# Performance work log

Hardware: AMD Instinct MI355X
Metric: run time of the kernel (lower is better)

Reference implementation:

```python
import jax, jax.numpy as jnp
import numpy as np

DIM = 512
HEADS = 8
DIM_HEAD = 64
INNER = HEADS * DIM_HEAD
B, N = 2, 2048
EPS = 1e-5


def setup_inputs() -> dict:
    key = jax.random.key(0)
    ks = jax.random.split(key, 7)
    x = jax.random.normal(ks[0], (B, N, DIM), dtype=jnp.float32)
    sph_dist = jax.random.uniform(ks[1], (N, N), dtype=jnp.float32)
    ln_g = jnp.ones((DIM,), jnp.float32) + 0.02 * jax.random.normal(ks[2], (DIM,))
    ln_b = 0.02 * jax.random.normal(ks[3], (DIM,))
    w_qkv = jax.random.normal(ks[4], (DIM, 3 * INNER), dtype=jnp.float32) / np.sqrt(DIM)
    w_out = jax.random.normal(ks[5], (INNER, DIM), dtype=jnp.float32) / np.sqrt(INNER)
    b_out = 0.02 * jax.random.normal(ks[6], (DIM,))
    return {"x": x, "sph_dist": sph_dist, "ln_g": ln_g, "ln_b": ln_b,
            "w_qkv": w_qkv, "w_out": w_out, "b_out": b_out}


def reference(x, sph_dist, ln_g, ln_b, w_qkv, w_out, b_out):
    scale = DIM_HEAD ** -0.5
    # LayerNorm over last dim
    mu = jnp.mean(x, axis=-1, keepdims=True)
    var = jnp.mean(jnp.square(x - mu), axis=-1, keepdims=True)
    xn = (x - mu) * jax.lax.rsqrt(var + EPS) * ln_g + ln_b
    # QKV projection -> [b, h, n, d]
    qkv = xn @ w_qkv  # [b, n, 3*inner]
    q, k, v = jnp.split(qkv, 3, axis=-1)
    split_heads = lambda t: t.reshape(B, N, HEADS, DIM_HEAD).transpose(0, 2, 1, 3)
    q, k, v = split_heads(q), split_heads(k), split_heads(v)
    dots = jnp.einsum('bhid,bhjd->bhij', q, k) * scale  # [b,h,n,n]
    dw = dots * (1.0 + sph_dist[None, None])
    # cross-head normalization: mean/std over head axis (std unbiased, ddof=1)
    m = jnp.mean(dw, axis=1, keepdims=True)
    sd = jnp.sqrt(jnp.sum(jnp.square(dw - m), axis=1, keepdims=True) / (HEADS - 1))
    dw = (dw - m) / sd
    attn = jax.nn.softmax(dw, axis=-1)
    out = jnp.einsum('bhij,bhjd->bhid', attn, v)
    out = out.transpose(0, 2, 1, 3).reshape(B, N, INNER)
    return out @ w_out + b_out
```

## Files before the change

kernel.cpp:

```cpp
#include <hip/hip_runtime.h>
#include <math.h>


typedef __attribute__((ext_vector_type(8))) short bf16x8;
typedef __attribute__((ext_vector_type(8))) unsigned short u16x8;
typedef __attribute__((ext_vector_type(4))) float f32x4;

constexpr int kDim = 512;
constexpr int kN = 2048;
constexpr float kEps = 1e-5f;
constexpr float kLog2e = 1.4426950408889634f;
constexpr float kShift2 = 2.6457513f * 1.4426950408889634f;

constexpr size_t OFF_XN    = 0;
constexpr size_t OFF_WQBT  = 4u << 20;
constexpr size_t OFF_WOHIT = 6u << 20;
constexpr size_t OFF_WOLOT = (6u << 20) + (512u << 10);
constexpr size_t OFF_QB    = 8u << 20;
constexpr size_t OFF_KHI   = 12u << 20;
constexpr size_t OFF_VTHI  = 16u << 20;
constexpr size_t OFF_OP    = 20u << 20;
constexpr size_t OP_STRIDE = 2097152;
constexpr size_t OFF_AOHI  = 0;
constexpr size_t OFF_AOLO  = 8u << 20;

__device__ __forceinline__ unsigned short bf16_rne(float f) {
  unsigned int u = __float_as_uint(f);
  u += 0x7fffu + ((u >> 16) & 1u);
  return (unsigned short)(u >> 16);
}
__device__ __forceinline__ void bf16_split(float x, unsigned short& hi,
                                           unsigned short& lo) {
  unsigned int u = __float_as_uint(x);
  hi = (unsigned short)(u >> 16);
  float r = x - __uint_as_float(u & 0xffff0000u);
  lo = (unsigned short)(__float_as_uint(r) >> 16);
}
__device__ __forceinline__ f32x4 mfma16(bf16x8 a, bf16x8 b, f32x4 c) {
  return __builtin_amdgcn_mfma_f32_16x16x32_bf16(a, b, c, 0, 0, 0);
}

__global__ __launch_bounds__(256) void k_prep(const float* __restrict__ x,
    const float* __restrict__ g, const float* __restrict__ bta,
    const float* __restrict__ wqkv, const float* __restrict__ wout,
    unsigned short* __restrict__ xn, unsigned short* __restrict__ wqbt,
    unsigned short* __restrict__ wohit, unsigned short* __restrict__ wolot) {
  __shared__ unsigned short th[64][72];
  __shared__ unsigned short tl[64][72];
  const int bid = blockIdx.x;
  const int t = threadIdx.x;
  if (bid < 1024) {
    const int row = bid * 4 + (t >> 6);
    const int lane = t & 63;
    const float* xr = x + (size_t)row * kDim + lane * 8;
    float4 a = *(const float4*)xr;
    float4 b = *(const float4*)(xr + 4);
    float s = a.x + a.y + a.z + a.w + b.x + b.y + b.z + b.w;
    float q = a.x*a.x + a.y*a.y + a.z*a.z + a.w*a.w
            + b.x*b.x + b.y*b.y + b.z*b.z + b.w*b.w;
#pragma unroll
    for (int off = 1; off < 64; off <<= 1) {
      s += __shfl_xor(s, off);
      q += __shfl_xor(q, off);
    }
    const float m = s * (1.0f / kDim);
    const float inv = rsqrtf(q * (1.0f / kDim) - m * m + kEps);
    float4 ga = *(const float4*)(g + lane * 8);
    float4 gb = *(const float4*)(g + lane * 8 + 4);
    float4 ba = *(const float4*)(bta + lane * 8);
    float4 bb = *(const float4*)(bta + lane * 8 + 4);
    u16x8 o;
    o[0] = bf16_rne((a.x - m) * inv * ga.x + ba.x);
    o[1] = bf16_rne((a.y - m) * inv * ga.y + ba.y);
    o[2] = bf16_rne((a.z - m) * inv * ga.z + ba.z);
    o[3] = bf16_rne((a.w - m) * inv * ga.w + ba.w);
    o[4] = bf16_rne((b.x - m) * inv * gb.x + bb.x);
    o[5] = bf16_rne((b.y - m) * inv * gb.y + bb.y);
    o[6] = bf16_rne((b.z - m) * inv * gb.z + bb.z);
    o[7] = bf16_rne((b.w - m) * inv * gb.w + bb.w);
    *(u16x8*)(xn + (size_t)row * kDim + lane * 8) = o;
  } else if (bid < 1216) {
    const int tid = bid - 1024;
    const int k0 = (tid / 24) * 64;
    const int n0 = (tid % 24) * 64;
    const int r = t >> 2, c0 = (t & 3) * 16;
    const float* src = wqkv + (size_t)(k0 + r) * 1536 + n0 + c0;
#pragma unroll
    for (int qq = 0; qq < 2; ++qq) {
      float4 v0 = *(const float4*)(src + qq * 8);
      float4 v1 = *(const float4*)(src + qq * 8 + 4);
      u16x8 o;
      o[0] = bf16_rne(v0.x); o[1] = bf16_rne(v0.y);
      o[2] = bf16_rne(v0.z); o[3] = bf16_rne(v0.w);
      o[4] = bf16_rne(v1.x); o[5] = bf16_rne(v1.y);
      o[6] = bf16_rne(v1.z); o[7] = bf16_rne(v1.w);
      *(u16x8*)&th[r][c0 + qq * 8] = o;
    }
    __syncthreads();
#pragma unroll
    for (int qq = 0; qq < 2; ++qq) {
      u16x8 o;
#pragma unroll
      for (int e = 0; e < 8; ++e) o[e] = th[c0 + qq * 8 + e][r];
      *(u16x8*)(wqbt + (size_t)(n0 + r) * 512 + k0 + c0 + qq * 8) = o;
    }
  } else {
    const int tid = bid - 1216;
    const int k0 = (tid >> 3) * 64;
    const int n0 = (tid & 7) * 64;
    const int r = t >> 2, c0 = (t & 3) * 16;
    const float* src = wout + (size_t)(k0 + r) * 512 + n0 + c0;
#pragma unroll
    for (int qq = 0; qq < 2; ++qq) {
      float4 v0 = *(const float4*)(src + qq * 8);
      float4 v1 = *(const float4*)(src + qq * 8 + 4);
      float e8[8] = {v0.x, v0.y, v0.z, v0.w, v1.x, v1.y, v1.z, v1.w};
      u16x8 oh, ol;
#pragma unroll
      for (int e = 0; e < 8; ++e) {
        unsigned short h2, l2;
        bf16_split(e8[e], h2, l2);
        oh[e] = h2;
        ol[e] = l2;
      }
      *(u16x8*)&th[r][c0 + qq * 8] = oh;
      *(u16x8*)&tl[r][c0 + qq * 8] = ol;
    }
    __syncthreads();
#pragma unroll
    for (int qq = 0; qq < 2; ++qq) {
      u16x8 oh, ol;
#pragma unroll
      for (int e = 0; e < 8; ++e) {
        oh[e] = th[c0 + qq * 8 + e][r];
        ol[e] = tl[c0 + qq * 8 + e][r];
      }
      *(u16x8*)(wohit + (size_t)(n0 + r) * 512 + k0 + c0 + qq * 8) = oh;
      *(u16x8*)(wolot + (size_t)(n0 + r) * 512 + k0 + c0 + qq * 8) = ol;
    }
  }
}

__global__ __launch_bounds__(256, 3) void k_gemm_qkv(
    const unsigned short* __restrict__ xn, const unsigned short* __restrict__ wqbt,
    unsigned short* __restrict__ qb, unsigned short* __restrict__ khi,
    unsigned short* __restrict__ vthi) {
  __shared__ unsigned short Ah[64 * 40];
  __shared__ unsigned short Bh[128 * 40];
  __shared__ unsigned short Vt[128 * 72];
  const int t = threadIdx.x;
  const int wv = t >> 6;
  const int lane = t & 63;
  const int col = lane & 15, gq = lane >> 4;
  const int lg = (blockIdx.x & 7) * 96 + (blockIdx.x >> 3);
  const int n0 = (lg % 12) * 128;
  const int m0 = (lg / 12) * 64;
  const int ar = t >> 2, aq = (t & 3) * 8;
  const int bnr = t >> 1, bko = (t & 1) * 16;

  f32x4 acc[8];
#pragma unroll
  for (int bn = 0; bn < 8; ++bn) acc[bn] = (f32x4){0.f, 0.f, 0.f, 0.f};

  for (int k0 = 0; k0 < kDim; k0 += 32) {
    *(u16x8*)&Ah[ar * 40 + aq] =
        *(const u16x8*)(xn + (size_t)(m0 + ar) * kDim + k0 + aq);
    {
      const unsigned short* wr = wqbt + (size_t)(n0 + bnr) * 512 + k0 + bko;
      *(u16x8*)&Bh[bnr * 40 + bko] = *(const u16x8*)(wr);
      *(u16x8*)&Bh[bnr * 40 + bko + 8] = *(const u16x8*)(wr + 8);
    }
    __syncthreads();
    bf16x8 ahf = *(const bf16x8*)&Ah[(wv * 16 + col) * 40 + gq * 8];
#pragma unroll
    for (int bn = 0; bn < 8; ++bn) {
      bf16x8 bhf = *(const bf16x8*)&Bh[(bn * 16 + col) * 40 + gq * 8];
      acc[bn] = mfma16(ahf, bhf, acc[bn]);
    }
    __syncthreads();
  }
  const int which = n0 >> 9;
  if (which < 2) {
    unsigned short* p = (which == 0) ? qb : khi;
#pragma unroll
    for (int r = 0; r < 4; ++r) {
      const int m = m0 + wv * 16 + gq * 4 + r;
      const int bI = m >> 11, nn = m & 2047;
#pragma unroll
      for (int bn = 0; bn < 8; ++bn) {
        const int cc = (n0 & 511) + bn * 16 + col;
        const int hh = cc >> 6, d = cc & 63;
        p[((size_t)(bI * 8 + hh) * kN + nn) * 64 + d] = bf16_rne(acc[bn][r]);
      }
    }
  } else {
#pragma unroll
    for (int bn = 0; bn < 8; ++bn)
#pragma unroll
      for (int r = 0; r < 4; ++r)
        Vt[(bn * 16 + col) * 72 + wv * 16 + gq * 4 + r] = bf16_rne(acc[bn][r]);
    __syncthreads();
    const int cl = t >> 1, mo = (t & 1) * 32;
    const int cc = (n0 & 511) + cl;
    const int hh = cc >> 6, d = cc & 63;
    const int bI = m0 >> 11, ntok = (m0 & 2047) + mo;
    unsigned short* dst = vthi + ((size_t)(bI * 8 + hh) * 64 + d) * kN + ntok;
#pragma unroll
    for (int e = 0; e < 4; ++e)
      *(u16x8*)(dst + e * 8) = *(const u16x8*)&Vt[cl * 72 + mo + e * 8];
  }
}

__global__ __launch_bounds__(512, 2) void k_attn(
    const unsigned short* __restrict__ qb, const unsigned short* __restrict__ khi,
    const unsigned short* __restrict__ vthi,
    float* __restrict__ op, float* __restrict__ lsum, int jLen) {
  constexpr int SSTR = 33;
  __shared__ float Ss[2][512 * SSTR];

  const int t = threadIdx.x;
  const int h = t >> 6;
  const int lane = t & 63;
  const int col = lane & 15;
  const int g = lane >> 4;
  const int lbid = (blockIdx.x & 7) * ((int)gridDim.x >> 3) + (blockIdx.x >> 3);
  const int tileId = lbid & 63;
  const int sId = lbid >> 6;
  const int bI = tileId >> 5;
  const int i0 = (tileId & 31) << 6;
  const int jStart = sId * jLen;
  int jEnd = jStart + jLen;
  if (jEnd > kN) jEnd = kN;
  const int ntile = (jEnd - jStart) >> 5;
  const size_t bh = (size_t)bI * 8 + h;
  float* opart = op + (size_t)sId * OP_STRIDE;

  bf16x8 qhf[4][2];
#pragma unroll
  for (int rb = 0; rb < 4; ++rb) {
    const size_t qoff = (bh * kN + i0 + rb * 16 + col) * 64 + g * 8;
    qhf[rb][0] = *(const bf16x8*)(qb + qoff);
    qhf[rb][1] = *(const bf16x8*)(qb + qoff + 32);
  }
  const unsigned short* kb_h = khi + (bh * kN + col) * 64 + g * 8;
  const unsigned short* vb_h = vthi + (bh * 64 + col) * kN + g * 8;

  const int iN = t >> 3;
  const int jN = (t & 7) * 4;

  f32x4 oacc[4][4];
#pragma unroll
  for (int rb = 0; rb < 4; ++rb)
#pragma unroll
    for (int nf = 0; nf < 4; ++nf) oacc[rb][nf] = (f32x4){0.f, 0.f, 0.f, 0.f};
  float lacc[8] = {0.f, 0.f, 0.f, 0.f, 0.f, 0.f, 0.f, 0.f};

  bf16x8 kh[2][2];
  auto load_k = [&](int j0) {
    const size_t ko = (size_t)j0 * 64;
#pragma unroll
    for (int jf = 0; jf < 2; ++jf)
#pragma unroll
      for (int c = 0; c < 2; ++c)
        kh[jf][c] = *(const bf16x8*)(kb_h + ko + jf * 1024 + c * 32);
  };
  auto qk_tile = [&](int buf) {
#pragma unroll
    for (int rb = 0; rb < 4; ++rb)
#pragma unroll
      for (int jf = 0; jf < 2; ++jf) {
        f32x4 a = (f32x4){0.f, 0.f, 0.f, 0.f};
        a = mfma16(qhf[rb][0], kh[jf][0], a);
        a = mfma16(qhf[rb][1], kh[jf][1], a);
#pragma unroll
        for (int r = 0; r < 4; ++r)
          Ss[buf][(h * 64 + rb * 16 + g * 4 + r) * SSTR + jf * 16 + col] = a[r];
      }
  };

  load_k(jStart);
  qk_tile(0);
  if (ntile > 1) load_k(jStart + 32);
  __syncthreads();

  for (int tt = 0; tt < ntile; ++tt) {
    const int cur = tt & 1;
    const int j0 = jStart + (tt << 5);
    if (tt + 1 < ntile) {
      qk_tile(cur ^ 1);
      if (tt + 2 < ntile) load_k(j0 + 64);
    }
    bf16x8 vhf[4];
#pragma unroll
    for (int nf = 0; nf < 4; ++nf)
      vhf[nf] = *(const bf16x8*)(vb_h + (size_t)(nf * 16) * kN + j0);
    {
      float dv[8][4];
#pragma unroll
      for (int hh = 0; hh < 8; ++hh) {
        float4 v = *(const float4*)&Ss[cur][(hh * 64 + iN) * SSTR + jN];
        dv[hh][0] = v.x; dv[hh][1] = v.y; dv[hh][2] = v.z; dv[hh][3] = v.w;
      }
#pragma unroll
      for (int jj = 0; jj < 4; ++jj) {
        float s = 0.f;
#pragma unroll
        for (int hh = 0; hh < 8; ++hh) s += dv[hh][jj];
        const float mean = s * 0.125f;
        float var = 0.f;
#pragma unroll
        for (int hh = 0; hh < 8; ++hh) {
          float d = dv[hh][jj] - mean;
          var += d * d;
        }
        const float inv2 = rsqrtf(var * (1.0f / 7.0f)) * kLog2e;
        const float base = mean * inv2 + kShift2;
#pragma unroll
        for (int hh = 0; hh < 8; ++hh)
          dv[hh][jj] = __builtin_amdgcn_exp2f(dv[hh][jj] * inv2 - base);
      }
#pragma unroll
      for (int hh = 0; hh < 8; ++hh) {
        lacc[hh] += (dv[hh][0] + dv[hh][1]) + (dv[hh][2] + dv[hh][3]);
        unsigned int p0 = (unsigned int)bf16_rne(dv[hh][0]) |
                          ((unsigned int)bf16_rne(dv[hh][1]) << 16);
        unsigned int p1 = (unsigned int)bf16_rne(dv[hh][2]) |
                          ((unsigned int)bf16_rne(dv[hh][3]) << 16);
        *(uint2*)((unsigned int*)&Ss[cur][(hh * 64 + iN) * SSTR] + (jN >> 1)) =
            make_uint2(p0, p1);
      }
    }
    __syncthreads();
    bf16x8 ph[4];
#pragma unroll
    for (int rb = 0; rb < 4; ++rb)
      ph[rb] = *(const bf16x8*)(
          (const unsigned int*)&Ss[cur][(h * 64 + rb * 16 + col) * SSTR] + g * 4);
#pragma unroll
    for (int rb = 0; rb < 4; ++rb)
#pragma unroll
      for (int nf = 0; nf < 4; ++nf)
        oacc[rb][nf] = mfma16(ph[rb], vhf[nf], oacc[rb][nf]);
    __syncthreads();
  }
#pragma unroll
  for (int off = 1; off < 8; off <<= 1)
#pragma unroll
    for (int hh = 0; hh < 8; ++hh) lacc[hh] += __shfl_xor(lacc[hh], off);
  if ((t & 7) == 0) {
#pragma unroll
    for (int hh = 0; hh < 8; ++hh)
      lsum[((size_t)sId * 16 + bI * 8 + hh) * kN + (i0 + iN)] = lacc[hh];
  }
#pragma unroll
  for (int rb = 0; rb < 4; ++rb) {
#pragma unroll
    for (int r = 0; r < 4; ++r) {
      float* dst = opart + ((size_t)bI * kN + i0 + rb * 16 + g * 4 + r) * 512 + h * 64;
#pragma unroll
      for (int nf = 0; nf < 4; ++nf)
        dst[nf * 16 + col] = oacc[rb][nf][r];
    }
  }
}

__global__ __launch_bounds__(256) void k_combine(const float* __restrict__ op,
    const float* __restrict__ lsum, int S,
    unsigned short* __restrict__ aohi, unsigned short* __restrict__ aolo) {
  const size_t e = ((size_t)blockIdx.x * 256 + threadIdx.x) * 4;
  const int row = (int)(e >> 9);
  const int col = (int)(e & 511);
  const int h = col >> 6;
  const int bI = row >> 11;
  const int n = row & 2047;
  const size_t base = (size_t)(bI * 8 + h) * kN + n;
  float L = 0.f;
  for (int s = 0; s < S; ++s) L += lsum[(size_t)s * 16 * kN + base];
  float4 acc = make_float4(0.f, 0.f, 0.f, 0.f);
  for (int s = 0; s < S; ++s) {
    float4 o4 = *(const float4*)(op + (size_t)s * OP_STRIDE + e);
    acc.x += o4.x; acc.y += o4.y; acc.z += o4.z; acc.w += o4.w;
  }
  const float inv = 1.0f / L;
  ushort4 hh, ll;
  bf16_split(acc.x * inv, hh.x, ll.x);
  bf16_split(acc.y * inv, hh.y, ll.y);
  bf16_split(acc.z * inv, hh.z, ll.z);
  bf16_split(acc.w * inv, hh.w, ll.w);
  *(ushort4*)(aohi + e) = hh;
  *(ushort4*)(aolo + e) = ll;
}

__global__ __launch_bounds__(256, 3) void k_gemm_out(
    const unsigned short* __restrict__ aohi, const unsigned short* __restrict__ aolo,
    const unsigned short* __restrict__ wohit, const unsigned short* __restrict__ wolot,
    const float* __restrict__ bias, float* __restrict__ out) {
  __shared__ unsigned short Ah[64 * 40], Al[64 * 40];
  __shared__ unsigned short Bh[128 * 40], Bl[128 * 40];
  const int t = threadIdx.x;
  const int wv = t >> 6;
  const int lane = t & 63;
  const int col = lane & 15, gq = lane >> 4;
  const int lg = (blockIdx.x & 7) * 32 + (blockIdx.x >> 3);
  const int n0 = (lg & 3) * 128;
  const int m0 = (lg >> 2) * 64;
  const int ar = t >> 2, aq = (t & 3) * 8;
  const int bnr = t >> 1, bko = (t & 1) * 16;

  f32x4 acc[8];
#pragma unroll
  for (int bn = 0; bn < 8; ++bn) acc[bn] = (f32x4){0.f, 0.f, 0.f, 0.f};

  for (int k0 = 0; k0 < 512; k0 += 32) {
    *(u16x8*)&Ah[ar * 40 + aq] =
        *(const u16x8*)(aohi + (size_t)(m0 + ar) * 512 + k0 + aq);
    *(u16x8*)&Al[ar * 40 + aq] =
        *(const u16x8*)(aolo + (size_t)(m0 + ar) * 512 + k0 + aq);
    {
      const unsigned short* wh = wohit + (size_t)(n0 + bnr) * 512 + k0 + bko;
      const unsigned short* wl = wolot + (size_t)(n0 + bnr) * 512 + k0 + bko;
      *(u16x8*)&Bh[bnr * 40 + bko] = *(const u16x8*)(wh);
      *(u16x8*)&Bh[bnr * 40 + bko + 8] = *(const u16x8*)(wh + 8);
      *(u16x8*)&Bl[bnr * 40 + bko] = *(const u16x8*)(wl);
      *(u16x8*)&Bl[bnr * 40 + bko + 8] = *(const u16x8*)(wl + 8);
    }
    __syncthreads();
    bf16x8 ahf = *(const bf16x8*)&Ah[(wv * 16 + col) * 40 + gq * 8];
    bf16x8 alf = *(const bf16x8*)&Al[(wv * 16 + col) * 40 + gq * 8];
#pragma unroll
    for (int bn = 0; bn < 8; ++bn) {
      bf16x8 bhf = *(const bf16x8*)&Bh[(bn * 16 + col) * 40 + gq * 8];
      bf16x8 blf = *(const bf16x8*)&Bl[(bn * 16 + col) * 40 + gq * 8];
      f32x4 aa = acc[bn];
      aa = mfma16(ahf, bhf, aa);
      aa = mfma16(alf, bhf, aa);
      aa = mfma16(ahf, blf, aa);
      acc[bn] = aa;
    }
    __syncthreads();
  }
  float bv[8];
#pragma unroll
  for (int bn = 0; bn < 8; ++bn) bv[bn] = bias[n0 + bn * 16 + col];
#pragma unroll
  for (int r = 0; r < 4; ++r) {
    const int m = m0 + wv * 16 + gq * 4 + r;
#pragma unroll
    for (int bn = 0; bn < 8; ++bn)
      out[(size_t)m * 512 + n0 + bn * 16 + col] = acc[bn][r] + bv[bn];
  }
}

extern "C" void kernel_launch(void* const* d_in, const int* in_sizes, int n_in,
                              void* d_out, int out_size, void* d_ws, size_t ws_size,
                              hipStream_t stream) {
  (void)in_sizes; (void)n_in; (void)out_size;
  const float* x    = (const float*)d_in[0];
  const float* g    = (const float*)d_in[2];
  const float* bta  = (const float*)d_in[3];
  const float* wqkv = (const float*)d_in[4];
  const float* wout = (const float*)d_in[5];
  const float* bout = (const float*)d_in[6];
  float* out = (float*)d_out;
  char* ws = (char*)d_ws;

  unsigned short* xn    = (unsigned short*)(ws + OFF_XN);
  unsigned short* wqbt  = (unsigned short*)(ws + OFF_WQBT);
  unsigned short* wohit = (unsigned short*)(ws + OFF_WOHIT);
  unsigned short* wolot = (unsigned short*)(ws + OFF_WOLOT);
  unsigned short* qb    = (unsigned short*)(ws + OFF_QB);
  unsigned short* khi   = (unsigned short*)(ws + OFF_KHI);
  unsigned short* vthi  = (unsigned short*)(ws + OFF_VTHI);
  unsigned short* aohi  = (unsigned short*)(ws + OFF_AOHI);
  unsigned short* aolo  = (unsigned short*)(ws + OFF_AOLO);
  float* op = (float*)(ws + OFF_OP);

  int S, jLen;
  if      (ws_size >= (54u << 20)) { S = 4; jLen = 512;  }
  else if (ws_size >= (46u << 20)) { S = 3; jLen = 704;  }
  else if (ws_size >= (37u << 20)) { S = 2; jLen = 1024; }
  else                             { S = 1; jLen = 2048; }
  float* lsum = (float*)(ws + OFF_OP + (size_t)S * OP_STRIDE * 4);

  k_prep<<<dim3(1280), dim3(256), 0, stream>>>(x, g, bta, wqkv, wout,
                                               xn, wqbt, wohit, wolot);
  k_gemm_qkv<<<dim3(768), dim3(256), 0, stream>>>(xn, wqbt, qb, khi, vthi);
  k_attn<<<dim3(64 * S), dim3(512), 0, stream>>>(qb, khi, vthi, op, lsum, jLen);
  k_combine<<<dim3(2048), dim3(256), 0, stream>>>(op, lsum, S, aohi, aolo);
  k_gemm_out<<<dim3(256), dim3(256), 0, stream>>>(aohi, aolo, wohit, wolot,
                                                  bout, out);
}
```

Measured before the change: 116.1 us.

## Use packed bf16 conversion and preload full B panel in QKV GEMM

Replaces the manual round-to-nearest bf16 bit manipulation with the packed hardware conversion intrinsic in the LayerNorm, weight-prep and attention softmax paths. This cuts ALU work in the hot attention inner loop. The QKV GEMM now loads its whole 128x512 weight panel into LDS once and reads the A operand straight from global memory, which removes the per-k-step shared staging and barriers. The large LDS footprint (about 150 KB) and launch bound of 1 lower occupancy, and A fragments now come from uncoalesced global reads.

After: 121.6 us. +4.8%, slower.

```diff
diff --git a/kernel.cpp b/kernel.cpp
--- a/kernel.cpp
+++ b/kernel.cpp
@@ -1,5 +1,7 @@
 #include <hip/hip_runtime.h>
+#include <hip/hip_bf16.h>
 #include <math.h>
+#include <string.h>
 
 
 typedef __attribute__((ext_vector_type(8))) short bf16x8;
@@ -35,6 +37,12 @@
   hi = (unsigned short)(u >> 16);
   float r = x - __uint_as_float(u & 0xffff0000u);
   lo = (unsigned short)(__float_as_uint(r) >> 16);
+}
+__device__ __forceinline__ unsigned int cvt_pk_bf16(float a, float b) {
+  __hip_bfloat162 h2 = __float22bfloat162_rn(make_float2(a, b));
+  unsigned int u;
+  memcpy(&u, &h2, 4);
+  return u;
 }
 __device__ __forceinline__ f32x4 mfma16(bf16x8 a, bf16x8 b, f32x4 c) {
   return __builtin_amdgcn_mfma_f32_16x16x32_bf16(a, b, c, 0, 0, 0);
@@ -69,16 +77,17 @@
     float4 gb = *(const float4*)(g + lane * 8 + 4);
     float4 ba = *(const float4*)(bta + lane * 8);
     float4 bb = *(const float4*)(bta + lane * 8 + 4);
-    u16x8 o;
-    o[0] = bf16_rne((a.x - m) * inv * ga.x + ba.x);
-    o[1] = bf16_rne((a.y - m) * inv * ga.y + ba.y);
-    o[2] = bf16_rne((a.z - m) * inv * ga.z + ba.z);
-    o[3] = bf16_rne((a.w - m) * inv * ga.w + ba.w);
-    o[4] = bf16_rne((b.x - m) * inv * gb.x + bb.x);
-    o[5] = bf16_rne((b.y - m) * inv * gb.y + bb.y);
-    o[6] = bf16_rne((b.z - m) * inv * gb.z + bb.z);
-    o[7] = bf16_rne((b.w - m) * inv * gb.w + bb.w);
-    *(u16x8*)(xn + (size_t)row * kDim + lane * 8) = o;
+    float e0 = (a.x - m) * inv * ga.x + ba.x;
+    float e1 = (a.y - m) * inv * ga.y + ba.y;
+    float e2 = (a.z - m) * inv * ga.z + ba.z;
+    float e3 = (a.w - m) * inv * ga.w + ba.w;
+    float e4 = (b.x - m) * inv * gb.x + bb.x;
+    float e5 = (b.y - m) * inv * gb.y + bb.y;
+    float e6 = (b.z - m) * inv * gb.z + bb.z;
+    float e7 = (b.w - m) * inv * gb.w + bb.w;
+    uint4 o = make_uint4(cvt_pk_bf16(e0, e1), cvt_pk_bf16(e2, e3),
+                         cvt_pk_bf16(e4, e5), cvt_pk_bf16(e6, e7));
+    *(uint4*)(xn + (size_t)row * kDim + lane * 8) = o;
   } else if (bid < 1216) {
     const int tid = bid - 1024;
     const int k0 = (tid / 24) * 64;
@@ -89,12 +98,9 @@
     for (int qq = 0; qq < 2; ++qq) {
       float4 v0 = *(const float4*)(src + qq * 8);
       float4 v1 = *(const float4*)(src + qq * 8 + 4);
-      u16x8 o;
-      o[0] = bf16_rne(v0.x); o[1] = bf16_rne(v0.y);
-      o[2] = bf16_rne(v0.z); o[3] = bf16_rne(v0.w);
-      o[4] = bf16_rne(v1.x); o[5] = bf16_rne(v1.y);
-      o[6] = bf16_rne(v1.z); o[7] = bf16_rne(v1.w);
-      *(u16x8*)&th[r][c0 + qq * 8] = o;
+      uint4 o = make_uint4(cvt_pk_bf16(v0.x, v0.y), cvt_pk_bf16(v0.z, v0.w),
+                           cvt_pk_bf16(v1.x, v1.y), cvt_pk_bf16(v1.z, v1.w));
+      *(uint4*)&th[r][c0 + qq * 8] = o;
     }
     __syncthreads();
 #pragma unroll
@@ -141,12 +147,12 @@
   }
 }
 
-__global__ __launch_bounds__(256, 3) void k_gemm_qkv(
+__global__ __launch_bounds__(256, 1) void k_gemm_qkv(
     const unsigned short* __restrict__ xn, const unsigned short* __restrict__ wqbt,
     unsigned short* __restrict__ qb, unsigned short* __restrict__ khi,
     unsigned short* __restrict__ vthi) {
-  __shared__ unsigned short Ah[64 * 40];
-  __shared__ unsigned short Bh[128 * 40];
+  constexpr int BSTR = 520;
+  __shared__ unsigned short BL[128 * BSTR];
   __shared__ unsigned short Vt[128 * 72];
   const int t = threadIdx.x;
   const int wv = t >> 6;
@@ -155,30 +161,34 @@
   const int lg = (blockIdx.x & 7) * 96 + (blockIdx.x >> 3);
   const int n0 = (lg % 12) * 128;
   const int m0 = (lg / 12) * 64;
-  const int ar = t >> 2, aq = (t & 3) * 8;
-  const int bnr = t >> 1, bko = (t & 1) * 16;
+
+  {
+    const int kk = (t & 31) * 16;
+#pragma unroll
+    for (int pass = 0; pass < 16; ++pass) {
+      const int r = pass * 8 + (t >> 5);
+      const unsigned short* src = wqbt + (size_t)(n0 + r) * 512 + kk;
+      *(u16x8*)&BL[r * BSTR + kk] = *(const u16x8*)(src);
+      *(u16x8*)&BL[r * BSTR + kk + 8] = *(const u16x8*)(src + 8);
+    }
+  }
+  __syncthreads();
 
   f32x4 acc[8];
 #pragma unroll
   for (int bn = 0; bn < 8; ++bn) acc[bn] = (f32x4){0.f, 0.f, 0.f, 0.f};
 
+  const unsigned short* ap = xn + (size_t)(m0 + wv * 16 + col) * kDim + gq * 8;
+#pragma unroll
   for (int k0 = 0; k0 < kDim; k0 += 32) {
-    *(u16x8*)&Ah[ar * 40 + aq] =
-        *(const u16x8*)(xn + (size_t)(m0 + ar) * kDim + k0 + aq);
-    {
-      const unsigned short* wr = wqbt + (size_t)(n0 + bnr) * 512 + k0 + bko;
-      *(u16x8*)&Bh[bnr * 40 + bko] = *(const u16x8*)(wr);
-      *(u16x8*)&Bh[bnr * 40 + bko + 8] = *(const u16x8*)(wr + 8);
-    }
-    __syncthreads();
-    bf16x8 ahf = *(const bf16x8*)&Ah[(wv * 16 + col) * 40 + gq * 8];
+    bf16x8 ahf = *(const bf16x8*)(ap + k0);
 #pragma unroll
     for (int bn = 0; bn < 8; ++bn) {
-      bf16x8 bhf = *(const bf16x8*)&Bh[(bn * 16 + col) * 40 + gq * 8];
+      bf16x8 bhf = *(const bf16x8*)&BL[(bn * 16 + col) * BSTR + k0 + gq * 8];
       acc[bn] = mfma16(ahf, bhf, acc[bn]);
     }
-    __syncthreads();
-  }
+  }
+
   const int which = n0 >> 9;
   if (which < 2) {
     unsigned short* p = (which == 0) ? qb : khi;
@@ -322,10 +332,8 @@
 #pragma unroll
       for (int hh = 0; hh < 8; ++hh) {
         lacc[hh] += (dv[hh][0] + dv[hh][1]) + (dv[hh][2] + dv[hh][3]);
-        unsigned int p0 = (unsigned int)bf16_rne(dv[hh][0]) |
-                          ((unsigned int)bf16_rne(dv[hh][1]) << 16);
-        unsigned int p1 = (unsigned int)bf16_rne(dv[hh][2]) |
-                          ((unsigned int)bf16_rne(dv[hh][3]) << 16);
+        unsigned int p0 = cvt_pk_bf16(dv[hh][0], dv[hh][1]);
+        unsigned int p1 = cvt_pk_bf16(dv[hh][2], dv[hh][3]);
         *(uint2*)((unsigned int*)&Ss[cur][(hh * 64 + iN) * SSTR] + (jN >> 1)) =
             make_uint2(p0, p1);
       }
```
